# Kernel optimization log

Hardware: AMD Instinct MI355X
Metric: run time of the kernel (lower is better)

Reference implementation:

```python
import jax, jax.numpy as jnp
import numpy as np

N_HEAD = 12
NEG_BIG = 1e10  # additive mask constant from the source


def setup_inputs() -> dict:
    key = jax.random.key(0)
    k1, k2, k3 = jax.random.split(key, 3)
    B, S, D = 8, 1024, 768
    x = jax.random.normal(k1, (B, S, D), dtype=jnp.float32)
    W_attn = jax.random.normal(k2, (D, 3 * D), dtype=jnp.float32) * 0.02
    W_proj = jax.random.normal(k3, (D, D), dtype=jnp.float32) * 0.02
    return {"x": x, "W_attn": W_attn, "W_proj": W_proj}


def reference(x, W_attn, W_proj):
    B, S, D = x.shape
    H = N_HEAD
    dh = D // H  # head dim = 64

    c = x @ W_attn                       # [B, S, 3D]
    q, k, v = jnp.split(c, 3, axis=-1)   # each [B, S, D]

    def split_heads(t):
        return t.reshape(B, S, H, dh).transpose(0, 2, 1, 3)  # [B, H, S, dh]

    q, k, v = split_heads(q), split_heads(k), split_heads(v)

    scale = 1.0 / jnp.sqrt(jnp.asarray(dh, q.dtype))
    a = jnp.einsum('bhqd,bhkd->bhqk', q, k) * scale  # [B, H, S, S]

    # causal mask: i >= j - ns + nd with nd == ns -> lower triangular
    i = jnp.arange(S)[:, None]
    j = jnp.arange(S)[None, :]
    m = (i >= j).astype(a.dtype)  # [S, S]
    a = a * m - (1.0 - m) * NEG_BIG

    a = jax.nn.softmax(a, axis=-1)

    out = jnp.einsum('bhqk,bhkd->bhqd', a, v)        # [B, H, S, dh]
    out = out.transpose(0, 2, 1, 3).reshape(B, S, D)  # merge heads
    return out @ W_proj
```

## Files before the change

kernel.cpp:

```cpp
#include <hip/hip_runtime.h>
#include <hip/hip_bf16.h>

typedef __attribute__((ext_vector_type(4))) float f32x4;
typedef __attribute__((ext_vector_type(8))) short short8;
typedef unsigned short u16;
typedef unsigned int u32;

__device__ __forceinline__ u16 f2bf(float f) {
    u32 u = __float_as_uint(f);
    u32 r = (u + 0x7fffu + ((u >> 16) & 1u)) >> 16;
    return (u16)r;
}
__device__ __forceinline__ u32 pack2bf(float a, float b) {
    __hip_bfloat162 w = __float22bfloat162_rn(float2{a, b});
    return *(u32*)&w;
}
__device__ __forceinline__ void stage16(const u16* gsrc, u16* ldsdst) {
    __builtin_amdgcn_global_load_lds((const __attribute__((address_space(1))) void*)gsrc,
                                     (__attribute__((address_space(3))) void*)ldsdst, 16, 0, 0);
}

__global__ __launch_bounds__(256) void prep(const float* __restrict__ x,
                                            const float* __restrict__ Wa,
                                            const float* __restrict__ Wp,
                                            u16* __restrict__ xb, u16* __restrict__ wat,
                                            u16* __restrict__ wpt) {
    __shared__ float tile[64][65];
    int blk = blockIdx.x;
    if (blk < 576) {
        const float* W;
        u16* Wt;
        int N, bx, by;
        if (blk < 432) {
            W = Wa; Wt = wat; N = 2304; bx = blk % 36; by = blk / 36;
        } else {
            int i = blk - 432;
            W = Wp; Wt = wpt; N = 768; bx = i % 12; by = i / 12;
        }
        int n0 = bx * 64, k0 = by * 64;
        int c = threadIdx.x & 63, r0 = threadIdx.x >> 6;
#pragma unroll
        for (int i = 0; i < 16; ++i) {
            int r = r0 * 16 + i;
            tile[r][c] = W[(size_t)(k0 + r) * N + n0 + c];
        }
        __syncthreads();
#pragma unroll
        for (int i = 0; i < 16; ++i) {
            int r = r0 * 16 + i;
            Wt[(size_t)(n0 + r) * 768 + k0 + c] = f2bf(tile[c][r]);
        }
    } else {
        const int n4 = (8 * 1024 * 768) / 4;
        int i = (blk - 576) * 256 + threadIdx.x;
        int stride = 1024 * 256;
        for (; i < n4; i += stride) {
            float4 v = ((const float4*)x)[i];
            ushort4 o;
            o.x = f2bf(v.x); o.y = f2bf(v.y); o.z = f2bf(v.z); o.w = f2bf(v.w);
            ((ushort4*)xb)[i] = o;
        }
    }
}

template <int MODE, int WM, int WN, int WPE>
__global__ __launch_bounds__(256, WPE) void gemmT(const u16* __restrict__ A,
                                                  const u16* __restrict__ Bt,
                                                  u16* __restrict__ q, u16* __restrict__ kk,
                                                  u16* __restrict__ v, float* __restrict__ outf,
                                                  int nby) {
    const int K = 768;
    const int BM = 2 * WM;
    const int BN = 2 * WN;
    const int NBF = WN / 16;
    __shared__ __align__(16) u16 As[BM * 64];
    __shared__ __align__(16) u16 Bs[BN * 64];
    int nwg = gridDim.x;
    int bid = blockIdx.x;
    int wgid = (bid & 7) * (nwg >> 3) + (bid >> 3);
    int mb = wgid / nby, nb = wgid % nby;
    int m0 = mb * BM, n0 = nb * BN;
    int tid = threadIdx.x;
    int wave = tid >> 6, lane = tid & 63;
    int lo = lane & 15, hi = lane >> 4;
    int wm = (wave >> 1) * WM, wn = (wave & 1) * WN;
    int srow = lane >> 3;
    int schunk = (lane & 7) ^ srow;
    int sw0 = (hi ^ (lo & 7)) * 8;
    int sw1 = ((4 + hi) ^ (lo & 7)) * 8;
    f32x4 acc[WM / 16][NBF] = {};
    const u16* Ab = A + (size_t)(m0 + (BM / 4) * wave + srow) * K + schunk * 8;
    const u16* Bb = Bt + (size_t)(n0 + (BN / 4) * wave + srow) * K + schunk * 8;
    u16* ldsA = &As[((BM / 4) * wave) * 64];
    u16* ldsB = &Bs[((BN / 4) * wave) * 64];

    for (int k0 = 0; k0 < K; k0 += 64) {
#pragma unroll
        for (int c = 0; c < BM / 32; ++c)
            stage16(Ab + k0 + (size_t)(8 * c) * K, ldsA + c * 512);
#pragma unroll
        for (int c = 0; c < BN / 32; ++c)
            stage16(Bb + k0 + (size_t)(8 * c) * K, ldsB + c * 512);
        __syncthreads();
#pragma unroll
        for (int ch = 0; ch < 2; ++ch) {
            int sw = ch ? sw1 : sw0;
            short8 af[WM / 16], bf[NBF];
#pragma unroll
            for (int i = 0; i < WM / 16; ++i)
                af[i] = *(const short8*)&As[(wm + 16 * i + lo) * 64 + sw];
#pragma unroll
            for (int j = 0; j < NBF; ++j)
                bf[j] = *(const short8*)&Bs[(wn + 16 * j + lo) * 64 + sw];
#pragma unroll
            for (int i = 0; i < WM / 16; ++i)
#pragma unroll
                for (int j = 0; j < NBF; ++j)
                    acc[i][j] = __builtin_amdgcn_mfma_f32_16x16x32_bf16(af[i], bf[j], acc[i][j], 0, 0, 0);
        }
        __syncthreads();
    }

    if (MODE == 0) {
        int ncb = n0 + wn;
        int which = ncb / 768;
        if (which == 2) {
#pragma unroll
            for (int i = 0; i < WM / 16; ++i) {
                int mrow = m0 + wm + 16 * i + 4 * hi;
                int b = mrow >> 10, s0 = mrow & 1023;
#pragma unroll
                for (int j = 0; j < NBF; ++j) {
                    int nc = (ncb % 768) + 16 * j;
                    int h = nc >> 6, d0 = nc & 63;
                    size_t bh = (size_t)(b * 12 + h);
                    uint2 pk;
                    pk.x = pack2bf(acc[i][j][0], acc[i][j][1]);
                    pk.y = pack2bf(acc[i][j][2], acc[i][j][3]);
                    *(uint2*)&v[(bh * 64 + d0 + lo) * 1024 + s0] = pk;
                }
            }
        } else {
            u16* dst = (which == 0) ? q : kk;
            float scale = (which == 0) ? 0.18033688f : 1.0f;
#pragma unroll
            for (int i = 0; i < WM / 16; ++i) {
#pragma unroll
                for (int r = 0; r < 4; ++r) {
                    int mrow = m0 + wm + 16 * i + 4 * hi + r;
                    int b = mrow >> 10, s = mrow & 1023;
#pragma unroll
                    for (int j = 0; j < NBF; ++j) {
                        int nc = (ncb % 768) + 16 * j;
                        int h = nc >> 6, d0 = nc & 63;
                        size_t bh = (size_t)(b * 12 + h);
                        dst[(bh * 1024 + s) * 64 + d0 + lo] = f2bf(acc[i][j][r] * scale);
                    }
                }
            }
        }
    } else {
#pragma unroll
        for (int i = 0; i < WM / 16; ++i)
#pragma unroll
            for (int j = 0; j < NBF; ++j)
#pragma unroll
                for (int r = 0; r < 4; ++r) {
                    int mrow = m0 + wm + 16 * i + 4 * hi + r;
                    int ncol = n0 + wn + 16 * j + lo;
                    outf[(size_t)mrow * 768 + ncol] = acc[i][j][r];
                }
    }
}

__global__ __launch_bounds__(256) void attn_fwd(const u16* __restrict__ qg,
                                                const u16* __restrict__ kg,
                                                const u16* __restrict__ vg,
                                                u16* __restrict__ ab) {
    __shared__ __align__(16) u16 Kl[2][64 * 64];
    __shared__ __align__(16) u16 Vl[2][64 * 64];
    __shared__ __align__(16) u16 P[4][16][72];
    int tid = threadIdx.x, wave = tid >> 6, lane = tid & 63;
    int lo = lane & 15, hi = lane >> 4;
    int bid = blockIdx.x;
    int j = bid >> 3;
    int bh = (bid & 7) * 12 + (j >> 3);
    int qp = j & 7;
    int b = bh / 12, h = bh % 12;
    u16(*Pw)[72] = P[wave];
    int srow = lane >> 3;
    int schunk = (lane & 7) ^ srow;
    const u16* kA = kg + ((size_t)bh << 16) + (size_t)(16 * wave + srow) * 64 + schunk * 8;
    const u16* vA = vg + ((size_t)bh << 16) + (size_t)(16 * wave + srow) * 1024 + schunk * 8;
    int sw0 = (hi ^ (lo & 7)) * 8;
    int sw1 = ((4 + hi) ^ (lo & 7)) * 8;

    auto stageKV = [&](int bufi, int kv0) {
        u16* kD = Kl[bufi] + wave * 1024;
        u16* vD = Vl[bufi] + wave * 1024;
        stage16(kA + (size_t)kv0 * 64, kD);
        stage16(kA + (size_t)kv0 * 64 + 512, kD + 512);
        stage16(vA + kv0, vD);
        stage16(vA + kv0 + 8 * 1024, vD + 512);
    };

#pragma unroll 1
    for (int part = 0; part < 2; ++part) {
        int qblk = part ? (15 - qp) : qp;
        int q0 = qblk * 64 + 16 * wave;
        const u16* qrow = qg + ((size_t)bh * 1024 + q0 + lo) * 64 + hi * 8;
        short8 qf0 = *(const short8*)qrow;
        short8 qf1 = *(const short8*)(qrow + 32);
        f32x4 acc[4] = {};
        float lsum = 0.f;
        int nt = qblk + 1;
        stageKV(0, 0);
        __syncthreads();
        int cur = 0;
#pragma unroll 1
        for (int t = 0; t < nt; ++t) {
            int kv0 = t * 64;
            if (t + 1 < nt) stageKV(cur ^ 1, kv0 + 64);
            f32x4 st[4] = {};
            __builtin_amdgcn_s_setprio(1);
#pragma unroll
            for (int f = 0; f < 4; ++f) {
                const u16* kp = &Kl[cur][(16 * f + lo) * 64];
                short8 k0 = *(const short8*)(kp + sw0);
                short8 k1 = *(const short8*)(kp + sw1);
                st[f] = __builtin_amdgcn_mfma_f32_16x16x32_bf16(k0, qf0, st[f], 0, 0, 0);
                st[f] = __builtin_amdgcn_mfma_f32_16x16x32_bf16(k1, qf1, st[f], 0, 0, 0);
            }
            __builtin_amdgcn_s_setprio(0);
            if (t == nt - 1) {
#pragma unroll
                for (int f = 0; f < 4; ++f) {
                    int kvb = kv0 + 16 * f + 4 * hi;
#pragma unroll
                    for (int r = 0; r < 4; ++r)
                        if (kvb + r > q0 + lo) st[f][r] = -1e30f;
                }
            }
#pragma unroll
            for (int f = 0; f < 4; ++f) {
                float p0 = exp2f(st[f][0]);
                float p1 = exp2f(st[f][1]);
                float p2 = exp2f(st[f][2]);
                float p3 = exp2f(st[f][3]);
                lsum += (p0 + p1) + (p2 + p3);
                uint2 wv;
                wv.x = pack2bf(p0, p1);
                wv.y = pack2bf(p2, p3);
                *(uint2*)&Pw[lo][16 * f + 4 * hi] = wv;
            }
            asm volatile("s_waitcnt lgkmcnt(0)" ::: "memory");
            __builtin_amdgcn_s_setprio(1);
#pragma unroll
            for (int c = 0; c < 2; ++c) {
                short8 pb = *(const short8*)&Pw[lo][c * 32 + hi * 8];
                int sw = c ? sw1 : sw0;
#pragma unroll
                for (int f2 = 0; f2 < 4; ++f2) {
                    short8 vf = *(const short8*)(&Vl[cur][(16 * f2 + lo) * 64] + sw);
                    acc[f2] = __builtin_amdgcn_mfma_f32_16x16x32_bf16(vf, pb, acc[f2], 0, 0, 0);
                }
            }
            __builtin_amdgcn_s_setprio(0);
            __syncthreads();
            cur ^= 1;
        }
        lsum += __shfl_xor(lsum, 16);
        lsum += __shfl_xor(lsum, 32);
        float inv = 1.0f / lsum;
        u16* orow = ab + ((size_t)b * 1024 + q0 + lo) * 768 + h * 64 + 4 * hi;
#pragma unroll
        for (int f2 = 0; f2 < 4; ++f2) {
            uint2 wv;
            wv.x = pack2bf(acc[f2][0] * inv, acc[f2][1] * inv);
            wv.y = pack2bf(acc[f2][2] * inv, acc[f2][3] * inv);
            *(uint2*)(orow + 16 * f2) = wv;
        }
    }
}

extern "C" void kernel_launch(void* const* d_in, const int* in_sizes, int n_in,
                              void* d_out, int out_size, void* d_ws, size_t ws_size,
                              hipStream_t stream) {
    const float* x = (const float*)d_in[0];
    const float* Wa = (const float*)d_in[1];
    const float* Wp = (const float*)d_in[2];
    float* out = (float*)d_out;
    char* ws = (char*)d_ws;
    const size_t SZ = (size_t)8 * 1024 * 768 * 2;
    u16* xb = (u16*)ws;
    u16* qb = (u16*)(ws + SZ);
    u16* kb = (u16*)(ws + 2 * SZ);
    u16* vb = (u16*)(ws + 3 * SZ);
    u16* ab = (u16*)(ws + 4 * SZ);
    u16* wat = (u16*)(ws + 5 * SZ);
    u16* wpt = (u16*)(ws + 5 * SZ + (size_t)2304 * 768 * 2);

    prep<<<1600, 256, 0, stream>>>(x, Wa, Wp, xb, wat, wpt);
    gemmT<0, 64, 96, 3><<<768, 256, 0, stream>>>(xb, wat, qb, kb, vb, nullptr, 12);
    attn_fwd<<<768, 256, 0, stream>>>(qb, kb, vb, ab);
    gemmT<1, 32, 64, 4><<<768, 256, 0, stream>>>(ab, wpt, nullptr, nullptr, nullptr, out, 6);
}
```

Before: 94.81 us.

## Load K/V fragments directly from global into registers, dropping LDS staging

The attention kernel stops staging K and V tiles through double-buffered shared memory with async global-to-LDS loads and block barriers. Each wave now loads its K and V MFMA fragments straight from global memory into registers every iteration, relying on L2/cache reuse across the four waves. The launch bounds also request 3 blocks per CU. This removes the block-wide barrier and the LDS traffic, but each wave now fetches the same K/V data redundantly and there is no explicit prefetch overlap.

New measurement: 152.7 us. 61.0% more time.

```diff
diff --git a/kernel.cpp b/kernel.cpp
--- a/kernel.cpp
+++ b/kernel.cpp
@@ -173,12 +173,10 @@
     }
 }
 
-__global__ __launch_bounds__(256) void attn_fwd(const u16* __restrict__ qg,
-                                                const u16* __restrict__ kg,
-                                                const u16* __restrict__ vg,
-                                                u16* __restrict__ ab) {
-    __shared__ __align__(16) u16 Kl[2][64 * 64];
-    __shared__ __align__(16) u16 Vl[2][64 * 64];
+__global__ __launch_bounds__(256, 3) void attn_fwd(const u16* __restrict__ qg,
+                                                   const u16* __restrict__ kg,
+                                                   const u16* __restrict__ vg,
+                                                   u16* __restrict__ ab) {
     __shared__ __align__(16) u16 P[4][16][72];
     int tid = threadIdx.x, wave = tid >> 6, lane = tid & 63;
     int lo = lane & 15, hi = lane >> 4;
@@ -188,21 +186,8 @@
     int qp = j & 7;
     int b = bh / 12, h = bh % 12;
     u16(*Pw)[72] = P[wave];
-    int srow = lane >> 3;
-    int schunk = (lane & 7) ^ srow;
-    const u16* kA = kg + ((size_t)bh << 16) + (size_t)(16 * wave + srow) * 64 + schunk * 8;
-    const u16* vA = vg + ((size_t)bh << 16) + (size_t)(16 * wave + srow) * 1024 + schunk * 8;
-    int sw0 = (hi ^ (lo & 7)) * 8;
-    int sw1 = ((4 + hi) ^ (lo & 7)) * 8;
-
-    auto stageKV = [&](int bufi, int kv0) {
-        u16* kD = Kl[bufi] + wave * 1024;
-        u16* vD = Vl[bufi] + wave * 1024;
-        stage16(kA + (size_t)kv0 * 64, kD);
-        stage16(kA + (size_t)kv0 * 64 + 512, kD + 512);
-        stage16(vA + kv0, vD);
-        stage16(vA + kv0 + 8 * 1024, vD + 512);
-    };
+    const u16* kptr = kg + ((size_t)bh << 16) + (size_t)lo * 64 + hi * 8;
+    const u16* vptr = vg + ((size_t)bh << 16) + (size_t)lo * 1024 + hi * 8;
 
 #pragma unroll 1
     for (int part = 0; part < 2; ++part) {
@@ -214,22 +199,28 @@
         f32x4 acc[4] = {};
         float lsum = 0.f;
         int nt = qblk + 1;
-        stageKV(0, 0);
-        __syncthreads();
-        int cur = 0;
 #pragma unroll 1
         for (int t = 0; t < nt; ++t) {
             int kv0 = t * 64;
-            if (t + 1 < nt) stageKV(cur ^ 1, kv0 + 64);
+            short8 kf[8], vf[8];
+#pragma unroll
+            for (int f = 0; f < 4; ++f) {
+                const u16* kp = kptr + (size_t)(kv0 + 16 * f) * 64;
+                kf[2 * f] = *(const short8*)kp;
+                kf[2 * f + 1] = *(const short8*)(kp + 32);
+            }
+#pragma unroll
+            for (int c = 0; c < 2; ++c)
+#pragma unroll
+                for (int f2 = 0; f2 < 4; ++f2)
+                    vf[c * 4 + f2] =
+                        *(const short8*)(vptr + (size_t)f2 * 16 * 1024 + kv0 + c * 32);
             f32x4 st[4] = {};
             __builtin_amdgcn_s_setprio(1);
 #pragma unroll
             for (int f = 0; f < 4; ++f) {
-                const u16* kp = &Kl[cur][(16 * f + lo) * 64];
-                short8 k0 = *(const short8*)(kp + sw0);
-                short8 k1 = *(const short8*)(kp + sw1);
-                st[f] = __builtin_amdgcn_mfma_f32_16x16x32_bf16(k0, qf0, st[f], 0, 0, 0);
-                st[f] = __builtin_amdgcn_mfma_f32_16x16x32_bf16(k1, qf1, st[f], 0, 0, 0);
+                st[f] = __builtin_amdgcn_mfma_f32_16x16x32_bf16(kf[2 * f], qf0, st[f], 0, 0, 0);
+                st[f] = __builtin_amdgcn_mfma_f32_16x16x32_bf16(kf[2 * f + 1], qf1, st[f], 0, 0, 0);
             }
             __builtin_amdgcn_s_setprio(0);
             if (t == nt - 1) {
@@ -258,16 +249,11 @@
 #pragma unroll
             for (int c = 0; c < 2; ++c) {
                 short8 pb = *(const short8*)&Pw[lo][c * 32 + hi * 8];
-                int sw = c ? sw1 : sw0;
-#pragma unroll
-                for (int f2 = 0; f2 < 4; ++f2) {
-                    short8 vf = *(const short8*)(&Vl[cur][(16 * f2 + lo) * 64] + sw);
-                    acc[f2] = __builtin_amdgcn_mfma_f32_16x16x32_bf16(vf, pb, acc[f2], 0, 0, 0);
-                }
+#pragma unroll
+                for (int f2 = 0; f2 < 4; ++f2)
+                    acc[f2] = __builtin_amdgcn_mfma_f32_16x16x32_bf16(vf[c * 4 + f2], pb, acc[f2], 0, 0, 0);
             }
             __builtin_amdgcn_s_setprio(0);
-            __syncthreads();
-            cur ^= 1;
         }
         lsum += __shfl_xor(lsum, 16);
         lsum += __shfl_xor(lsum, 32);
```

## Give each attention block one query tile and drop K/V double buffering

Applied to the files above, without the earlier changes.

The attention kernel no longer processes a paired short and long query block per workgroup. It launches 1536 blocks, each handling a single query tile, ordered longest-first within each XCD. K/V staging becomes single-buffered with a barrier before compute, which halves LDS use so more blocks can be resident. In exchange it loses the overlap of the next tile's loads with current compute and relies on hardware scheduling rather than pairing to balance the causal workload.

After: 92.84 us (median of 2 runs). 2.1% less time.

```diff
diff --git a/kernel.cpp b/kernel.cpp
--- a/kernel.cpp
+++ b/kernel.cpp
@@ -177,15 +177,16 @@
                                                 const u16* __restrict__ kg,
                                                 const u16* __restrict__ vg,
                                                 u16* __restrict__ ab) {
-    __shared__ __align__(16) u16 Kl[2][64 * 64];
-    __shared__ __align__(16) u16 Vl[2][64 * 64];
+    __shared__ __align__(16) u16 Kl[64 * 64];
+    __shared__ __align__(16) u16 Vl[64 * 64];
     __shared__ __align__(16) u16 P[4][16][72];
     int tid = threadIdx.x, wave = tid >> 6, lane = tid & 63;
     int lo = lane & 15, hi = lane >> 4;
     int bid = blockIdx.x;
-    int j = bid >> 3;
-    int bh = (bid & 7) * 12 + (j >> 3);
-    int qp = j & 7;
+    int xcd = bid & 7;
+    int idx = bid >> 3;
+    int qblk = 15 - (idx / 12);
+    int bh = xcd * 12 + (idx % 12);
     int b = bh / 12, h = bh % 12;
     u16(*Pw)[72] = P[wave];
     int srow = lane >> 3;
@@ -195,91 +196,84 @@
     int sw0 = (hi ^ (lo & 7)) * 8;
     int sw1 = ((4 + hi) ^ (lo & 7)) * 8;
 
-    auto stageKV = [&](int bufi, int kv0) {
-        u16* kD = Kl[bufi] + wave * 1024;
-        u16* vD = Vl[bufi] + wave * 1024;
+    auto stageKV = [&](int kv0) {
+        u16* kD = Kl + wave * 1024;
+        u16* vD = Vl + wave * 1024;
         stage16(kA + (size_t)kv0 * 64, kD);
         stage16(kA + (size_t)kv0 * 64 + 512, kD + 512);
         stage16(vA + kv0, vD);
         stage16(vA + kv0 + 8 * 1024, vD + 512);
     };
 
+    int q0 = qblk * 64 + 16 * wave;
+    const u16* qrow = qg + ((size_t)bh * 1024 + q0 + lo) * 64 + hi * 8;
+    short8 qf0 = *(const short8*)qrow;
+    short8 qf1 = *(const short8*)(qrow + 32);
+    f32x4 acc[4] = {};
+    float lsum = 0.f;
+    int nt = qblk + 1;
 #pragma unroll 1
-    for (int part = 0; part < 2; ++part) {
-        int qblk = part ? (15 - qp) : qp;
-        int q0 = qblk * 64 + 16 * wave;
-        const u16* qrow = qg + ((size_t)bh * 1024 + q0 + lo) * 64 + hi * 8;
-        short8 qf0 = *(const short8*)qrow;
-        short8 qf1 = *(const short8*)(qrow + 32);
-        f32x4 acc[4] = {};
-        float lsum = 0.f;
-        int nt = qblk + 1;
-        stageKV(0, 0);
-        __syncthreads();
-        int cur = 0;
-#pragma unroll 1
-        for (int t = 0; t < nt; ++t) {
-            int kv0 = t * 64;
-            if (t + 1 < nt) stageKV(cur ^ 1, kv0 + 64);
-            f32x4 st[4] = {};
-            __builtin_amdgcn_s_setprio(1);
+    for (int t = 0; t < nt; ++t) {
+        int kv0 = t * 64;
+        stageKV(kv0);
+        __syncthreads();
+        f32x4 st[4] = {};
+        __builtin_amdgcn_s_setprio(1);
+#pragma unroll
+        for (int f = 0; f < 4; ++f) {
+            const u16* kp = &Kl[(16 * f + lo) * 64];
+            short8 k0 = *(const short8*)(kp + sw0);
+            short8 k1 = *(const short8*)(kp + sw1);
+            st[f] = __builtin_amdgcn_mfma_f32_16x16x32_bf16(k0, qf0, st[f], 0, 0, 0);
+            st[f] = __builtin_amdgcn_mfma_f32_16x16x32_bf16(k1, qf1, st[f], 0, 0, 0);
+        }
+        __builtin_amdgcn_s_setprio(0);
+        if (t == nt - 1) {
 #pragma unroll
             for (int f = 0; f < 4; ++f) {
-                const u16* kp = &Kl[cur][(16 * f + lo) * 64];
-                short8 k0 = *(const short8*)(kp + sw0);
-                short8 k1 = *(const short8*)(kp + sw1);
-                st[f] = __builtin_amdgcn_mfma_f32_16x16x32_bf16(k0, qf0, st[f], 0, 0, 0);
-                st[f] = __builtin_amdgcn_mfma_f32_16x16x32_bf16(k1, qf1, st[f], 0, 0, 0);
+                int kvb = kv0 + 16 * f + 4 * hi;
+#pragma unroll
+                for (int r = 0; r < 4; ++r)
+                    if (kvb + r > q0 + lo) st[f][r] = -1e30f;
             }
-            __builtin_amdgcn_s_setprio(0);
-            if (t == nt - 1) {
-#pragma unroll
-                for (int f = 0; f < 4; ++f) {
-                    int kvb = kv0 + 16 * f + 4 * hi;
-#pragma unroll
-                    for (int r = 0; r < 4; ++r)
-                        if (kvb + r > q0 + lo) st[f][r] = -1e30f;
-                }
+        }
+#pragma unroll
+        for (int f = 0; f < 4; ++f) {
+            float p0 = exp2f(st[f][0]);
+            float p1 = exp2f(st[f][1]);
+            float p2 = exp2f(st[f][2]);
+            float p3 = exp2f(st[f][3]);
+            lsum += (p0 + p1) + (p2 + p3);
+            uint2 wv;
+            wv.x = pack2bf(p0, p1);
+            wv.y = pack2bf(p2, p3);
+            *(uint2*)&Pw[lo][16 * f + 4 * hi] = wv;
+        }
+        asm volatile("s_waitcnt lgkmcnt(0)" ::: "memory");
+        __builtin_amdgcn_s_setprio(1);
+#pragma unroll
+        for (int c = 0; c < 2; ++c) {
+            short8 pb = *(const short8*)&Pw[lo][c * 32 + hi * 8];
+            int sw = c ? sw1 : sw0;
+#pragma unroll
+            for (int f2 = 0; f2 < 4; ++f2) {
+                short8 vf = *(const short8*)(&Vl[(16 * f2 + lo) * 64] + sw);
+                acc[f2] = __builtin_amdgcn_mfma_f32_16x16x32_bf16(vf, pb, acc[f2], 0, 0, 0);
             }
-#pragma unroll
-            for (int f = 0; f < 4; ++f) {
-                float p0 = exp2f(st[f][0]);
-                float p1 = exp2f(st[f][1]);
-                float p2 = exp2f(st[f][2]);
-                float p3 = exp2f(st[f][3]);
-                lsum += (p0 + p1) + (p2 + p3);
-                uint2 wv;
-                wv.x = pack2bf(p0, p1);
-                wv.y = pack2bf(p2, p3);
-                *(uint2*)&Pw[lo][16 * f + 4 * hi] = wv;
-            }
-            asm volatile("s_waitcnt lgkmcnt(0)" ::: "memory");
-            __builtin_amdgcn_s_setprio(1);
-#pragma unroll
-            for (int c = 0; c < 2; ++c) {
-                short8 pb = *(const short8*)&Pw[lo][c * 32 + hi * 8];
-                int sw = c ? sw1 : sw0;
-#pragma unroll
-                for (int f2 = 0; f2 < 4; ++f2) {
-                    short8 vf = *(const short8*)(&Vl[cur][(16 * f2 + lo) * 64] + sw);
-                    acc[f2] = __builtin_amdgcn_mfma_f32_16x16x32_bf16(vf, pb, acc[f2], 0, 0, 0);
-                }
-            }
-            __builtin_amdgcn_s_setprio(0);
-            __syncthreads();
-            cur ^= 1;
-        }
-        lsum += __shfl_xor(lsum, 16);
-        lsum += __shfl_xor(lsum, 32);
-        float inv = 1.0f / lsum;
-        u16* orow = ab + ((size_t)b * 1024 + q0 + lo) * 768 + h * 64 + 4 * hi;
-#pragma unroll
-        for (int f2 = 0; f2 < 4; ++f2) {
-            uint2 wv;
-            wv.x = pack2bf(acc[f2][0] * inv, acc[f2][1] * inv);
-            wv.y = pack2bf(acc[f2][2] * inv, acc[f2][3] * inv);
-            *(uint2*)(orow + 16 * f2) = wv;
-        }
+        }
+        __builtin_amdgcn_s_setprio(0);
+        __syncthreads();
+    }
+    lsum += __shfl_xor(lsum, 16);
+    lsum += __shfl_xor(lsum, 32);
+    float inv = 1.0f / lsum;
+    u16* orow = ab + ((size_t)b * 1024 + q0 + lo) * 768 + h * 64 + 4 * hi;
+#pragma unroll
+    for (int f2 = 0; f2 < 4; ++f2) {
+        uint2 wv;
+        wv.x = pack2bf(acc[f2][0] * inv, acc[f2][1] * inv);
+        wv.y = pack2bf(acc[f2][2] * inv, acc[f2][3] * inv);
+        *(uint2*)(orow + 16 * f2) = wv;
     }
 }
 
@@ -302,6 +296,6 @@
 
     prep<<<1600, 256, 0, stream>>>(x, Wa, Wp, xb, wat, wpt);
     gemmT<0, 64, 96, 3><<<768, 256, 0, stream>>>(xb, wat, qb, kb, vb, nullptr, 12);
-    attn_fwd<<<768, 256, 0, stream>>>(qb, kb, vb, ab);
+    attn_fwd<<<1536, 256, 0, stream>>>(qb, kb, vb, ab);
     gemmT<1, 32, 64, 4><<<768, 256, 0, stream>>>(ab, wpt, nullptr, nullptr, nullptr, out, 6);
 }
```
